# Kernel optimization log

Hardware: AMD Instinct MI355X
Metric: run time of the kernel (lower is better)

Reference implementation:

```python
import jax, jax.numpy as jnp
import numpy as np

NUM_ATOM_TYPE = 120
NUM_CHIRALITY_TAG = 3
NUM_BOND_TYPE = 6
NUM_BOND_DIRECTION = 3
EMB_DIM = 300
FEAT_DIM = 256
NUM_LAYER = 5
NUM_GRAPHS = 2048
OUT_DIM = 2  # classification: output_dim(1) * 2
BN_EPS = 1e-5


def setup_inputs() -> dict:
    key = jax.random.key(0)
    ks = jax.random.split(key, 20)
    N, E = 100000, 200000
    x = jax.random.randint(ks[0], (N, 2), 0, 3, dtype=jnp.int64) if jax.config.jax_enable_x64 else jax.random.randint(ks[0], (N, 2), 0, 3, dtype=jnp.int32)
    edge_index = jax.random.randint(ks[1], (2, E), 0, N, dtype=x.dtype)
    edge_attr = jax.random.randint(ks[2], (E, 2), 0, 3, dtype=x.dtype)
    batch = jnp.sort(jax.random.randint(ks[3], (N,), 0, NUM_GRAPHS, dtype=x.dtype))
    f32 = jnp.float32
    return {
        'x': x, 'edge_index': edge_index, 'edge_attr': edge_attr, 'batch': batch,
        'x_emb1': jax.random.normal(ks[4], (NUM_ATOM_TYPE, EMB_DIM), f32) * 0.1,
        'x_emb2': jax.random.normal(ks[5], (NUM_CHIRALITY_TAG, EMB_DIM), f32) * 0.1,
        'conv_w': jax.random.normal(ks[6], (NUM_LAYER, EMB_DIM, EMB_DIM), f32) * (1.0 / np.sqrt(EMB_DIM)),
        'conv_b': jnp.zeros((NUM_LAYER, EMB_DIM), f32),
        'eemb1': jax.random.normal(ks[7], (NUM_LAYER, NUM_BOND_TYPE, 1), f32) * 0.1,
        'eemb2': jax.random.normal(ks[8], (NUM_LAYER, NUM_BOND_DIRECTION, 1), f32) * 0.1,
        'bn_gamma': jnp.ones((NUM_LAYER, EMB_DIM), f32),
        'bn_beta': jnp.zeros((NUM_LAYER, EMB_DIM), f32),
        'feat_w': jax.random.normal(ks[9], (EMB_DIM, FEAT_DIM), f32) * (1.0 / np.sqrt(EMB_DIM)),
        'feat_b': jnp.zeros((FEAT_DIM,), f32),
        'pred_w1': jax.random.normal(ks[10], (FEAT_DIM, FEAT_DIM // 2), f32) * (1.0 / np.sqrt(FEAT_DIM)),
        'pred_b1': jnp.zeros((FEAT_DIM // 2,), f32),
        'pred_w2': jax.random.normal(ks[11], (FEAT_DIM // 2, OUT_DIM), f32) * (1.0 / np.sqrt(FEAT_DIM // 2)),
        'pred_b2': jnp.zeros((OUT_DIM,), f32),
    }


def reference(x, edge_index, edge_attr, batch, x_emb1, x_emb2, conv_w, conv_b,
              eemb1, eemb2, bn_gamma, bn_beta, feat_w, feat_b,
              pred_w1, pred_b1, pred_w2, pred_b2):
    N = x.shape[0]
    # add self loops (same for every layer)
    loop = jnp.arange(N, dtype=edge_index.dtype)
    src = jnp.concatenate([edge_index[0], loop])            # [E+N]
    dst = jnp.concatenate([edge_index[1], loop])            # [E+N]
    # self-loop edge attr: bond type 4, direction 0
    ea0 = jnp.concatenate([edge_attr[:, 0], jnp.full((N,), 4, edge_attr.dtype)])
    ea1 = jnp.concatenate([edge_attr[:, 1], jnp.zeros((N,), edge_attr.dtype)])

    h = x_emb1[x[:, 0]] + x_emb2[x[:, 1]]                   # [N, emb_dim]
    for l in range(NUM_LAYER):
        e = eemb1[l][ea0] + eemb2[l][ea1]                   # [E+N, 1]
        hw = h @ conv_w[l]                                  # [N, emb_dim]
        msg = hw[src] + e                                   # gather + broadcast-add
        out = jax.ops.segment_sum(msg, dst, num_segments=N) + conv_b[l]
        # BatchNorm1d (training-mode batch stats, biased variance)
        mean = jnp.mean(out, axis=0)
        var = jnp.mean((out - mean) ** 2, axis=0)
        out = (out - mean) * jax.lax.rsqrt(var + BN_EPS) * bn_gamma[l] + bn_beta[l]
        h = jax.nn.relu(out)                                # dropout p=0

    h = h @ feat_w + feat_b                                 # [N, feat_dim]
    # global mean pool per graph
    sums = jax.ops.segment_sum(h, batch, num_segments=NUM_GRAPHS)
    counts = jax.ops.segment_sum(jnp.ones((N,), h.dtype), batch, num_segments=NUM_GRAPHS)
    g = sums / jnp.maximum(counts, 1.0)[:, None]            # [G, feat_dim]
    pred = jax.nn.relu(g @ pred_w1 + pred_b1) @ pred_w2 + pred_b2
    return (g, pred)
```

## Files before the change

### kernel.cpp

```cpp
#include <hip/hip_runtime.h>
#include <math.h>

#define EMB 300
#define KP 320
#define FEAT 256
#define NLAYER 5
#define NGRAPH 2048
#define BNEPS 1e-5f
#define SCAN_B 256
#define NPART 64
#define CH 40

typedef __attribute__((ext_vector_type(8))) short short8;
typedef __attribute__((ext_vector_type(8))) unsigned short ushort8;
typedef __attribute__((ext_vector_type(4))) float f32x4;

#define GLOAD_LDS16(src, dst) __builtin_amdgcn_global_load_lds( \
    (const __attribute__((address_space(1))) unsigned int*)(const void*)(src), \
    (__attribute__((address_space(3))) unsigned int*)(void*)(dst), 16, 0, 0)

static __device__ __forceinline__ unsigned short f2bf(float f) {
    unsigned int u = __float_as_uint(f);
    unsigned int r = (u + 0x7FFFu + ((u >> 16) & 1u)) >> 16;
    return (unsigned short)r;
}
static __device__ __forceinline__ float bf2f(unsigned short h) {
    return __uint_as_float(((unsigned int)h) << 16);
}

__global__ void k_prepW(const float* __restrict__ convw, const float* __restrict__ featw,
                        unsigned short* __restrict__ whi) {
    int idx = blockIdx.x * 256 + threadIdx.x;
    if (idx >= 1856 * KP) return;
    int row = idx / KP;
    int k = idx - row * KP;
    float w = 0.f;
    if (row < 1600) {
        int l = row / KP;
        int c = row - l * KP;
        if (c < EMB && k < EMB) w = convw[(size_t)l * EMB * EMB + (size_t)k * EMB + c];
    } else {
        int c = row - 1600;
        if (k < EMB) w = featw[(size_t)k * FEAT + c];
    }
    whi[idx] = f2bf(w);
}

__global__ void k_s_all(const int* __restrict__ ei, const int* __restrict__ ea,
                        const float* __restrict__ eemb1, const float* __restrict__ eemb2,
                        float* __restrict__ s, int N, int E) {
    int t = blockIdx.x * blockDim.x + threadIdx.x;
    int total = E + N;
    if (t >= total) return;
    if (t < E) {
        int d = ei[E + t];
        int a0 = ea[2 * t], a1 = ea[2 * t + 1];
        for (int l = 0; l < NLAYER; ++l) {
            float v = eemb1[l * 6 + a0] + eemb2[l * 3 + a1];
            atomicAdd(&s[(size_t)l * N + d], v);
        }
    } else {
        int v = t - E;
        for (int l = 0; l < NLAYER; ++l) {
            float val = eemb1[l * 6 + 4] + eemb2[l * 3 + 0];
            atomicAdd(&s[(size_t)l * N + v], val);
        }
    }
}

__global__ void k_count(const int* __restrict__ ei, int* __restrict__ deg, int E) {
    int e = blockIdx.x * blockDim.x + threadIdx.x;
    if (e < E) atomicAdd(&deg[ei[E + e]], 1);
}

__global__ void k_scanA(const int* __restrict__ deg, int* __restrict__ bsum, int N) {
    __shared__ int sm[SCAN_B];
    int i = blockIdx.x * SCAN_B + threadIdx.x;
    sm[threadIdx.x] = (i < N) ? deg[i] : 0;
    __syncthreads();
    for (int off = SCAN_B / 2; off > 0; off >>= 1) {
        if (threadIdx.x < off) sm[threadIdx.x] += sm[threadIdx.x + off];
        __syncthreads();
    }
    if (threadIdx.x == 0) bsum[blockIdx.x] = sm[0];
}

__global__ void k_scanB(int* __restrict__ bsum, int nb, int* __restrict__ rowptr, int N) {
    if (threadIdx.x == 0 && blockIdx.x == 0) {
        int acc = 0;
        for (int i = 0; i < nb; ++i) { int v = bsum[i]; bsum[i] = acc; acc += v; }
        rowptr[N] = acc;
    }
}

__global__ void k_scanC(const int* __restrict__ deg, const int* __restrict__ bsum,
                        int* __restrict__ rowptr, int N) {
    __shared__ int sm[SCAN_B];
    int i = blockIdx.x * SCAN_B + threadIdx.x;
    int v = (i < N) ? deg[i] : 0;
    sm[threadIdx.x] = v;
    __syncthreads();
    for (int off = 1; off < SCAN_B; off <<= 1) {
        int add = (threadIdx.x >= off) ? sm[threadIdx.x - off] : 0;
        __syncthreads();
        sm[threadIdx.x] += add;
        __syncthreads();
    }
    if (i < N) rowptr[i] = bsum[blockIdx.x] + sm[threadIdx.x] - v;
}

__global__ void k_scatter(const int* __restrict__ ei, const int* __restrict__ rowptr,
                          int* __restrict__ cursor, int* __restrict__ esrc, int E) {
    int e = blockIdx.x * blockDim.x + threadIdx.x;
    if (e >= E) return;
    int d = ei[E + e], srcv = ei[e];
    int p = atomicAdd(&cursor[d], 1);
    esrc[rowptr[d] + p] = srcv;
}

__global__ void k_h0(const int* __restrict__ x, const float* __restrict__ emb1,
                     const float* __restrict__ emb2, unsigned short* __restrict__ h0, int N) {
    int idx = blockIdx.x * 256 + threadIdx.x;
    if (idx >= N * 160) return;
    int v = idx / 160, fp = idx - v * 160;
    unsigned int out = 0;
    if (fp < 150) {
        int f = fp * 2;
        size_t b1 = (size_t)x[2 * v] * EMB + f;
        size_t b2 = (size_t)x[2 * v + 1] * EMB + f;
        float a = emb1[b1] + emb2[b2];
        float b = emb1[b1 + 1] + emb2[b2 + 1];
        out = (unsigned int)f2bf(a) | ((unsigned int)f2bf(b) << 16);
    }
    *(unsigned int*)(h0 + (size_t)v * KP + fp * 2) = out;
}

template <bool BN>
__global__ __launch_bounds__(256) void k_aggV(
    const unsigned short* __restrict__ Prev, const int* __restrict__ rowptr,
    const int* __restrict__ esrc,
    const float* __restrict__ scale, const float* __restrict__ shift,
    unsigned short* __restrict__ A, int N) {
    int idx = blockIdx.x * 256 + threadIdx.x;
    if (idx >= N * CH) return;
    int row = idx / CH, c = idx - row * CH;

    f32x4 s0, s1, t0, t1;
    if constexpr (BN) {
        s0 = *(const f32x4*)(scale + c * 8);
        s1 = *(const f32x4*)(scale + c * 8 + 4);
        t0 = *(const f32x4*)(shift + c * 8);
        t1 = *(const f32x4*)(shift + c * 8 + 4);
    }
    int rs = rowptr[row], re = rowptr[row + 1];

    float f[8];
    ushort8 u = *(const ushort8*)(Prev + (size_t)row * KP + c * 8);
#pragma unroll
    for (int e = 0; e < 4; ++e) {
        if constexpr (BN) {
            f[e]     = fmaxf(fmaf(bf2f(u[e]), s0[e], t0[e]), 0.f);
            f[e + 4] = fmaxf(fmaf(bf2f(u[e + 4]), s1[e], t1[e]), 0.f);
        } else {
            f[e] = bf2f(u[e]);
            f[e + 4] = bf2f(u[e + 4]);
        }
    }
    int ii = rs;
    int un = (ii < re) ? esrc[ii] : 0;
    while (ii < re) {
        int ucur = un;
        ++ii;
        if (ii < re) un = esrc[ii];
        ushort8 uu = *(const ushort8*)(Prev + (size_t)ucur * KP + c * 8);
#pragma unroll
        for (int e = 0; e < 4; ++e) {
            if constexpr (BN) {
                f[e]     += fmaxf(fmaf(bf2f(uu[e]), s0[e], t0[e]), 0.f);
                f[e + 4] += fmaxf(fmaf(bf2f(uu[e + 4]), s1[e], t1[e]), 0.f);
            } else {
                f[e] += bf2f(uu[e]);
                f[e + 4] += bf2f(uu[e + 4]);
            }
        }
    }
    short8 v;
#pragma unroll
    for (int e = 0; e < 8; ++e) v[e] = (short)f2bf(f[e]);
    *(short8*)(A + (size_t)row * KP + c * 8) = v;
}

template <int COLF, int BMT, bool BN>
__global__ __launch_bounds__(256, 2) void k_mm(
    const unsigned short* __restrict__ Prev,
    const float* __restrict__ scale, const float* __restrict__ shift,
    const unsigned short* __restrict__ Whi,
    const float* __restrict__ bias, const float* __restrict__ svec,
    unsigned short* __restrict__ OutB,
    float* __restrict__ partsum, float* __restrict__ partsq, int N) {
    __shared__ unsigned short As[BMT * KP];
    constexpr int WSTR = (COLF == 5) ? KP : FEAT;
    constexpr int RF = BMT / 16;
    constexpr int NCHUNK = BMT * CH;
    int tid = threadIdx.x;
    int row0 = blockIdx.x * BMT;
    int wave = tid >> 6, lane = tid & 63;

    if constexpr (!BN) {
#pragma unroll
        for (int it = 0; it < NCHUNK / 256; ++it) {
            int base = it * 256 + wave * 64;
            int idx = base + lane;
            int r = idx / CH, c = idx - r * CH;
            const unsigned short* src =
                Prev + (size_t)(row0 + r) * KP + (size_t)(c ^ (r & 7)) * 8;
            GLOAD_LDS16(src, &As[(size_t)base * 8]);
        }
    } else {
        for (int idx = tid; idx < NCHUNK; idx += 256) {
            int r = idx / CH, c = idx - r * CH;
            int row = row0 + r;
            short8 v = (short8){0, 0, 0, 0, 0, 0, 0, 0};
            if (row < N) {
                ushort8 u = *(const ushort8*)(Prev + (size_t)row * KP + c * 8);
                f32x4 s0 = *(const f32x4*)(scale + c * 8);
                f32x4 s1 = *(const f32x4*)(scale + c * 8 + 4);
                f32x4 t0 = *(const f32x4*)(shift + c * 8);
                f32x4 t1 = *(const f32x4*)(shift + c * 8 + 4);
#pragma unroll
                for (int e = 0; e < 4; ++e) {
                    v[e]     = (short)f2bf(fmaxf(fmaf(bf2f(u[e]), s0[e], t0[e]), 0.f));
                    v[e + 4] = (short)f2bf(fmaxf(fmaf(bf2f(u[e + 4]), s1[e], t1[e]), 0.f));
                }
            }
            *(short8*)&As[(size_t)(r * CH + (c ^ (r & 7))) * 8] = v;
        }
    }
    __syncthreads();

    int q = lane >> 4, m = lane & 15;
    int wbase = wave * (COLF * 16);

    f32x4 acc[RF][COLF];
#pragma unroll
    for (int rf = 0; rf < RF; ++rf)
#pragma unroll
        for (int cf = 0; cf < COLF; ++cf)
            acc[rf][cf] = (f32x4){0.f, 0.f, 0.f, 0.f};

    size_t woff[COLF];
#pragma unroll
    for (int cf = 0; cf < COLF; ++cf)
        woff[cf] = (size_t)(wbase + cf * 16 + m) * KP;

#pragma unroll 2
    for (int ks = 0; ks < 10; ++ks) {
        short8 a[RF];
#pragma unroll
        for (int rf = 0; rf < RF; ++rf) {
            int r = rf * 16 + m;
            int ch = ks * 4 + q;
            a[rf] = *(const short8*)&As[(size_t)(r * CH + (ch ^ (r & 7))) * 8];
        }
        int kb = ks * 32 + q * 8;
#pragma unroll
        for (int cf = 0; cf < COLF; ++cf) {
            short8 bh = *(const short8*)(Whi + woff[cf] + kb);
#pragma unroll
            for (int rf = 0; rf < RF; ++rf) {
                acc[rf][cf] = __builtin_amdgcn_mfma_f32_16x16x32_bf16(a[rf], bh, acc[rf][cf], 0, 0, 0);
            }
        }
    }

    __syncthreads();

    if constexpr (COLF == 5) {
        float sv[RF][4];
#pragma unroll
        for (int rf = 0; rf < RF; ++rf)
#pragma unroll
            for (int i = 0; i < 4; ++i) {
                int row = row0 + rf * 16 + q * 4 + i;
                sv[rf][i] = (row < N) ? svec[row] : 0.f;
            }
        int part = blockIdx.x & (NPART - 1);
#pragma unroll
        for (int cf = 0; cf < COLF; ++cf) {
            int col = wbase + cf * 16 + m;
            bool cok = col < EMB;
            float bia = cok ? bias[col] : 0.f;
            float lsum = 0.f, lsq = 0.f;
#pragma unroll
            for (int rf = 0; rf < RF; ++rf)
#pragma unroll
                for (int i = 0; i < 4; ++i) {
                    int r = rf * 16 + q * 4 + i;
                    int row = row0 + r;
                    float val = 0.f;
                    if (cok && row < N) {
                        val = acc[rf][cf][i] + bia + sv[rf][i];
                        lsum += val; lsq += val * val;
                    }
                    As[(size_t)r * WSTR + col] = f2bf(val);
                }
            lsum += __shfl_xor(lsum, 16); lsum += __shfl_xor(lsum, 32);
            lsq  += __shfl_xor(lsq, 16);  lsq  += __shfl_xor(lsq, 32);
            if (q == 0 && cok) {
                atomicAdd(&partsum[(size_t)part * KP + col], lsum);
                atomicAdd(&partsq[(size_t)part * KP + col], lsq);
            }
        }
    } else {
#pragma unroll
        for (int cf = 0; cf < COLF; ++cf) {
            int col = wbase + cf * 16 + m;
            float bia = bias[col];
#pragma unroll
            for (int rf = 0; rf < RF; ++rf)
#pragma unroll
                for (int i = 0; i < 4; ++i) {
                    int r = rf * 16 + q * 4 + i;
                    As[(size_t)r * WSTR + col] = f2bf(acc[rf][cf][i] + bia);
                }
        }
    }
    __syncthreads();

    unsigned short* dst = OutB + (size_t)row0 * WSTR;
    for (int idx = tid; idx < BMT * WSTR / 8; idx += 256) {
        *(short8*)(dst + (size_t)idx * 8) = *(const short8*)&As[(size_t)idx * 8];
    }
}

__global__ void k_bnfin(const float* __restrict__ partsum, const float* __restrict__ partsq,
                        const float* __restrict__ gamma, const float* __restrict__ beta,
                        float* __restrict__ scale, float* __restrict__ shift, int N) {
    int j = threadIdx.x;
    if (j >= KP) return;
    if (j < EMB) {
        float s = 0.f, sq = 0.f;
        for (int p = 0; p < NPART; ++p) { s += partsum[p * KP + j]; sq += partsq[p * KP + j]; }
        float invN = 1.0f / (float)N;
        float mean = s * invN;
        float var = sq * invN - mean * mean;
        float sc = gamma[j] * rsqrtf(var + BNEPS);
        scale[j] = sc;
        shift[j] = beta[j] - mean * sc;
    } else {
        scale[j] = 0.f;
        shift[j] = 0.f;
    }
}

__global__ void k_counts(const int* __restrict__ batch, float* __restrict__ counts, int N) {
    int i = blockIdx.x * blockDim.x + threadIdx.x;
    if (i < N) atomicAdd(&counts[batch[i]], 1.0f);
}

#define PROWS 128
__global__ __launch_bounds__(256) void k_pool(const unsigned short* __restrict__ H,
                                              const int* __restrict__ batch,
                                              float* __restrict__ gsums, int N) {
    int j = threadIdx.x;
    int r0 = blockIdx.x * PROWS;
    int rend = min(r0 + PROWS, N);
    float run = 0.f;
    int curg = -1;
    for (int r = r0; r < rend; ++r) {
        int g = batch[r];
        if (g != curg) {
            if (curg >= 0) atomicAdd(&gsums[(size_t)curg * FEAT + j], run);
            curg = g; run = 0.f;
        }
        run += bf2f(H[(size_t)r * FEAT + j]);
    }
    if (curg >= 0) atomicAdd(&gsums[(size_t)curg * FEAT + j], run);
}

__global__ void k_poolfin(const float* __restrict__ gsums, const float* __restrict__ counts,
                          float* __restrict__ gout) {
    int i = blockIdx.x * blockDim.x + threadIdx.x;
    if (i >= NGRAPH * FEAT) return;
    int g = i / FEAT;
    gout[i] = gsums[i] / fmaxf(counts[g], 1.0f);
}

__global__ __launch_bounds__(128) void k_pred(
    const float* __restrict__ gout, const float* __restrict__ w1, const float* __restrict__ b1,
    const float* __restrict__ w2, const float* __restrict__ b2, float* __restrict__ pout) {
    __shared__ float gs[FEAT];
    __shared__ float h1[128];
    int g = blockIdx.x;
    for (int k = threadIdx.x; k < FEAT; k += 128) gs[k] = gout[(size_t)g * FEAT + k];
    __syncthreads();
    int j = threadIdx.x;
    float acc = b1[j];
    for (int k = 0; k < FEAT; ++k) acc = fmaf(gs[k], w1[(size_t)k * 128 + j], acc);
    h1[j] = fmaxf(acc, 0.f);
    __syncthreads();
    if (j < 2) {
        float acc2 = b2[j];
        for (int k = 0; k < 128; ++k) acc2 = fmaf(h1[k], w2[k * 2 + j], acc2);
        pout[(size_t)g * 2 + j] = acc2;
    }
}

extern "C" void kernel_launch(void* const* d_in, const int* in_sizes, int n_in,
                              void* d_out, int out_size, void* d_ws, size_t ws_size,
                              hipStream_t stream) {
    const int* x      = (const int*)d_in[0];
    const int* ei     = (const int*)d_in[1];
    const int* ea     = (const int*)d_in[2];
    const int* batch  = (const int*)d_in[3];
    const float* xemb1 = (const float*)d_in[4];
    const float* xemb2 = (const float*)d_in[5];
    const float* convw = (const float*)d_in[6];
    const float* convb = (const float*)d_in[7];
    const float* eemb1 = (const float*)d_in[8];
    const float* eemb2 = (const float*)d_in[9];
    const float* gamma = (const float*)d_in[10];
    const float* beta  = (const float*)d_in[11];
    const float* featw = (const float*)d_in[12];
    const float* featb = (const float*)d_in[13];
    const float* pw1   = (const float*)d_in[14];
    const float* pb1   = (const float*)d_in[15];
    const float* pw2   = (const float*)d_in[16];
    const float* pb2   = (const float*)d_in[17];

    int N = in_sizes[0] / 2;
    int E = in_sizes[1] / 2;
    int nrbF = (N + 127) / 128;
    size_t Npad = (size_t)nrbF * 128;
    int nrbC = (int)(Npad / 64);

    char* p = (char*)d_ws;
    auto alloc = [&](size_t bytes) { char* r = p; p += (bytes + 255) & ~255ull; return r; };
    unsigned short* H0Hf = (unsigned short*)alloc(Npad * KP * 2);
    unsigned short* Abf  = (unsigned short*)alloc(Npad * KP * 2);
    unsigned short* OutB = (unsigned short*)alloc(Npad * KP * 2);
    float* sAll    = (float*)alloc((size_t)NLAYER * N * 4);
    float* partsum = (float*)alloc((size_t)NLAYER * NPART * KP * 4);
    float* partsq  = (float*)alloc((size_t)NLAYER * NPART * KP * 4);
    char*  zero1_end = p;
    float* scaleA  = (float*)alloc((size_t)NLAYER * KP * 4);
    float* shiftA  = (float*)alloc((size_t)NLAYER * KP * 4);
    unsigned short* Whi = (unsigned short*)alloc((size_t)1856 * KP * 2);
    int*   deg    = (int*)alloc((size_t)N * 4);
    int*   rowptr = (int*)alloc((size_t)(N + 1) * 4);
    int*   cursor = (int*)alloc((size_t)N * 4);
    char*  zero2_end = p;
    int*   esrc   = (int*)alloc((size_t)E * 4);
    float* gsums  = (float*)alloc((size_t)NGRAPH * FEAT * 4);
    float* counts = (float*)alloc(NGRAPH * 4);
    char*  zero3_end = p;
    int nb = (N + SCAN_B - 1) / SCAN_B;
    int*   bsum   = (int*)alloc((size_t)nb * 4);

    hipMemsetAsync(sAll, 0, (size_t)(zero1_end - (char*)sAll), stream);
    hipMemsetAsync(deg, 0, (size_t)(zero2_end - (char*)deg), stream);
    hipMemsetAsync(gsums, 0, (size_t)(zero3_end - (char*)gsums), stream);
    if (Npad > (size_t)N)
        hipMemsetAsync(Abf + (size_t)N * KP, 0, (Npad - (size_t)N) * KP * 2, stream);

    int tpb = 256;
    k_prepW<<<(1856 * KP + 255) / 256, 256, 0, stream>>>(convw, featw, Whi);
    k_s_all<<<(E + N + tpb - 1) / tpb, tpb, 0, stream>>>(ei, ea, eemb1, eemb2, sAll, N, E);
    k_count<<<(E + tpb - 1) / tpb, tpb, 0, stream>>>(ei, deg, E);
    k_scanA<<<nb, SCAN_B, 0, stream>>>(deg, bsum, N);
    k_scanB<<<1, 64, 0, stream>>>(bsum, nb, rowptr, N);
    k_scanC<<<nb, SCAN_B, 0, stream>>>(deg, bsum, rowptr, N);
    k_scatter<<<(E + tpb - 1) / tpb, tpb, 0, stream>>>(ei, rowptr, cursor, esrc, E);
    k_h0<<<(N * 160 + 255) / 256, 256, 0, stream>>>(x, xemb1, xemb2, H0Hf, N);

    int gagg = (N * CH + 255) / 256;
    k_aggV<false><<<gagg, 256, 0, stream>>>(H0Hf, rowptr, esrc, nullptr, nullptr, Abf, N);

    for (int l = 0; l < NLAYER; ++l) {
        k_mm<5, 64, false><<<nrbC, 256, 0, stream>>>(
            Abf, nullptr, nullptr,
            Whi + (size_t)l * KP * KP,
            convb + (size_t)l * EMB, sAll + (size_t)l * N,
            OutB,
            partsum + (size_t)l * NPART * KP, partsq + (size_t)l * NPART * KP, N);
        k_bnfin<<<1, 320, 0, stream>>>(
            partsum + (size_t)l * NPART * KP, partsq + (size_t)l * NPART * KP,
            gamma + (size_t)l * EMB, beta + (size_t)l * EMB,
            scaleA + (size_t)l * KP, shiftA + (size_t)l * KP, N);
        if (l < NLAYER - 1)
            k_aggV<true><<<gagg, 256, 0, stream>>>(OutB, rowptr, esrc,
                                                   scaleA + (size_t)l * KP, shiftA + (size_t)l * KP,
                                                   Abf, N);
    }

    k_mm<4, 128, true><<<nrbF, 256, 0, stream>>>(
        OutB, scaleA + (size_t)4 * KP, shiftA + (size_t)4 * KP,
        Whi + (size_t)1600 * KP,
        featb, nullptr,
        H0Hf, nullptr, nullptr, N);

    float* gout = (float*)d_out;
    float* pout = gout + (size_t)NGRAPH * FEAT;
    k_counts<<<(N + tpb - 1) / tpb, tpb, 0, stream>>>(batch, counts, N);
    k_pool<<<(N + PROWS - 1) / PROWS, 256, 0, stream>>>(H0Hf, batch, gsums, N);
    k_poolfin<<<(NGRAPH * FEAT + tpb - 1) / tpb, tpb, 0, stream>>>(gsums, counts, gout);
    k_pred<<<NGRAPH, 128, 0, stream>>>(gout, pw1, pb1, pw2, pb2, pout);
}
```

Measured before the change: 895.9 us.

## Widen aggregation per-thread chunks, enlarge conv GEMM row tile, parallelize BN reduction

The aggregation kernel now has each thread handle 16 features (two 16-byte loads per neighbor) instead of 8. This halves the thread count and the repeated rowptr/esrc index loads per row. The conv-layer GEMM switches from 64-row to 128-row tiles, doubling LDS use and per-thread accumulators while halving block count. The single-block BN finalize kernel is replaced by a 320-block kernel that reduces the 64 partials per feature with wave shuffles. Wider aggregation threads may lower occupancy and memory-level parallelism, and larger GEMM tiles reduce the number of blocks available to fill the CUs.

```diff
diff --git a/kernel.cpp b/kernel.cpp
--- a/kernel.cpp
+++ b/kernel.cpp
@@ -10,6 +10,7 @@
 #define SCAN_B 256
 #define NPART 64
 #define CH 40
+#define CHW 20
 
 typedef __attribute__((ext_vector_type(8))) short short8;
 typedef __attribute__((ext_vector_type(8))) unsigned short ushort8;
@@ -142,28 +143,34 @@
     const float* __restrict__ scale, const float* __restrict__ shift,
     unsigned short* __restrict__ A, int N) {
     int idx = blockIdx.x * 256 + threadIdx.x;
-    if (idx >= N * CH) return;
-    int row = idx / CH, c = idx - row * CH;
-
-    f32x4 s0, s1, t0, t1;
+    if (idx >= N * CHW) return;
+    int row = idx / CHW, c = idx - row * CHW;
+    int f0 = c * 16;
+
+    f32x4 sc[4], sh[4];
     if constexpr (BN) {
-        s0 = *(const f32x4*)(scale + c * 8);
-        s1 = *(const f32x4*)(scale + c * 8 + 4);
-        t0 = *(const f32x4*)(shift + c * 8);
-        t1 = *(const f32x4*)(shift + c * 8 + 4);
+#pragma unroll
+        for (int g = 0; g < 4; ++g) {
+            sc[g] = *(const f32x4*)(scale + f0 + g * 4);
+            sh[g] = *(const f32x4*)(shift + f0 + g * 4);
+        }
     }
     int rs = rowptr[row], re = rowptr[row + 1];
 
-    float f[8];
-    ushort8 u = *(const ushort8*)(Prev + (size_t)row * KP + c * 8);
-#pragma unroll
-    for (int e = 0; e < 4; ++e) {
-        if constexpr (BN) {
-            f[e]     = fmaxf(fmaf(bf2f(u[e]), s0[e], t0[e]), 0.f);
-            f[e + 4] = fmaxf(fmaf(bf2f(u[e + 4]), s1[e], t1[e]), 0.f);
-        } else {
-            f[e] = bf2f(u[e]);
-            f[e + 4] = bf2f(u[e + 4]);
+    float f[16];
+    {
+        const unsigned short* pr = Prev + (size_t)row * KP + f0;
+        ushort8 u0 = *(const ushort8*)pr;
+        ushort8 u1 = *(const ushort8*)(pr + 8);
+#pragma unroll
+        for (int e = 0; e < 8; ++e) {
+            if constexpr (BN) {
+                f[e]     = fmaxf(fmaf(bf2f(u0[e]), sc[e >> 2][e & 3], sh[e >> 2][e & 3]), 0.f);
+                f[e + 8] = fmaxf(fmaf(bf2f(u1[e]), sc[2 + (e >> 2)][e & 3], sh[2 + (e >> 2)][e & 3]), 0.f);
+            } else {
+                f[e] = bf2f(u0[e]);
+                f[e + 8] = bf2f(u1[e]);
+            }
         }
     }
     int ii = rs;
@@ -172,22 +179,29 @@
         int ucur = un;
         ++ii;
         if (ii < re) un = esrc[ii];
-        ushort8 uu = *(const ushort8*)(Prev + (size_t)ucur * KP + c * 8);
-#pragma unroll
-        for (int e = 0; e < 4; ++e) {
+        const unsigned short* pu = Prev + (size_t)ucur * KP + f0;
+        ushort8 uu0 = *(const ushort8*)pu;
+        ushort8 uu1 = *(const ushort8*)(pu + 8);
+#pragma unroll
+        for (int e = 0; e < 8; ++e) {
             if constexpr (BN) {
-                f[e]     += fmaxf(fmaf(bf2f(uu[e]), s0[e], t0[e]), 0.f);
-                f[e + 4] += fmaxf(fmaf(bf2f(uu[e + 4]), s1[e], t1[e]), 0.f);
+                f[e]     += fmaxf(fmaf(bf2f(uu0[e]), sc[e >> 2][e & 3], sh[e >> 2][e & 3]), 0.f);
+                f[e + 8] += fmaxf(fmaf(bf2f(uu1[e]), sc[2 + (e >> 2)][e & 3], sh[2 + (e >> 2)][e & 3]), 0.f);
             } else {
-                f[e] += bf2f(uu[e]);
-                f[e + 4] += bf2f(uu[e + 4]);
+                f[e] += bf2f(uu0[e]);
+                f[e + 8] += bf2f(uu1[e]);
             }
         }
     }
-    short8 v;
-#pragma unroll
-    for (int e = 0; e < 8; ++e) v[e] = (short)f2bf(f[e]);
-    *(short8*)(A + (size_t)row * KP + c * 8) = v;
+    short8 v0, v1;
+#pragma unroll
+    for (int e = 0; e < 8; ++e) {
+        v0[e] = (short)f2bf(f[e]);
+        v1[e] = (short)f2bf(f[e + 8]);
+    }
+    unsigned short* dst = A + (size_t)row * KP + f0;
+    *(short8*)dst = v0;
+    *(short8*)(dst + 8) = v1;
 }
 
 template <int COLF, int BMT, bool BN>
@@ -333,23 +347,30 @@
     }
 }
 
-__global__ void k_bnfin(const float* __restrict__ partsum, const float* __restrict__ partsq,
-                        const float* __restrict__ gamma, const float* __restrict__ beta,
-                        float* __restrict__ scale, float* __restrict__ shift, int N) {
-    int j = threadIdx.x;
-    if (j >= KP) return;
-    if (j < EMB) {
-        float s = 0.f, sq = 0.f;
-        for (int p = 0; p < NPART; ++p) { s += partsum[p * KP + j]; sq += partsq[p * KP + j]; }
+__global__ __launch_bounds__(64) void k_bnred(
+    const float* __restrict__ partsum, const float* __restrict__ partsq,
+    const float* __restrict__ gamma, const float* __restrict__ beta,
+    float* __restrict__ scale, float* __restrict__ shift, int N) {
+    int j = blockIdx.x;
+    int p = threadIdx.x;
+    if (j >= EMB) {
+        if (p == 0) { scale[j] = 0.f; shift[j] = 0.f; }
+        return;
+    }
+    float s = partsum[(size_t)p * KP + j];
+    float sq = partsq[(size_t)p * KP + j];
+#pragma unroll
+    for (int off = 32; off > 0; off >>= 1) {
+        s += __shfl_down(s, off);
+        sq += __shfl_down(sq, off);
+    }
+    if (p == 0) {
         float invN = 1.0f / (float)N;
         float mean = s * invN;
         float var = sq * invN - mean * mean;
         float sc = gamma[j] * rsqrtf(var + BNEPS);
         scale[j] = sc;
         shift[j] = beta[j] - mean * sc;
-    } else {
-        scale[j] = 0.f;
-        shift[j] = 0.f;
     }
 }
 
@@ -430,9 +451,8 @@
 
     int N = in_sizes[0] / 2;
     int E = in_sizes[1] / 2;
-    int nrbF = (N + 127) / 128;
-    size_t Npad = (size_t)nrbF * 128;
-    int nrbC = (int)(Npad / 64);
+    int nrb = (N + 127) / 128;
+    size_t Npad = (size_t)nrb * 128;
 
     char* p = (char*)d_ws;
     auto alloc = [&](size_t bytes) { char* r = p; p += (bytes + 255) & ~255ull; return r; };
@@ -473,17 +493,17 @@
     k_scatter<<<(E + tpb - 1) / tpb, tpb, 0, stream>>>(ei, rowptr, cursor, esrc, E);
     k_h0<<<(N * 160 + 255) / 256, 256, 0, stream>>>(x, xemb1, xemb2, H0Hf, N);
 
-    int gagg = (N * CH + 255) / 256;
+    int gagg = (N * CHW + 255) / 256;
     k_aggV<false><<<gagg, 256, 0, stream>>>(H0Hf, rowptr, esrc, nullptr, nullptr, Abf, N);
 
     for (int l = 0; l < NLAYER; ++l) {
-        k_mm<5, 64, false><<<nrbC, 256, 0, stream>>>(
+        k_mm<5, 128, false><<<nrb, 256, 0, stream>>>(
             Abf, nullptr, nullptr,
             Whi + (size_t)l * KP * KP,
             convb + (size_t)l * EMB, sAll + (size_t)l * N,
             OutB,
             partsum + (size_t)l * NPART * KP, partsq + (size_t)l * NPART * KP, N);
-        k_bnfin<<<1, 320, 0, stream>>>(
+        k_bnred<<<KP, 64, 0, stream>>>(
             partsum + (size_t)l * NPART * KP, partsq + (size_t)l * NPART * KP,
             gamma + (size_t)l * EMB, beta + (size_t)l * EMB,
             scaleA + (size_t)l * KP, shiftA + (size_t)l * KP, N);
@@ -493,7 +513,7 @@
                                                    Abf, N);
     }
 
-    k_mm<4, 128, true><<<nrbF, 256, 0, stream>>>(
+    k_mm<4, 128, true><<<nrb, 256, 0, stream>>>(
         OutB, scaleA + (size_t)4 * KP, shiftA + (size_t)4 * KP,
         Whi + (size_t)1600 * KP,
         featb, nullptr,
```

New measurement: 811.0 us. 9.5% less time.
